# Kernel tuning notes

Hardware: AMD Instinct MI355X
Metric: run time of the kernel (lower is better)

## Reference

```python
import jax, jax.numpy as jnp
import numpy as np

DIM = 256
HEADS = 8
HEAD_DIM = DIM // HEADS
WS = 7            # window size
SHIFT = 3         # shift size
H = 56
W = 56
B = 32
WA = WS * WS      # window area = 49
NWH, NWW = H // WS, W // WS
NW = NWH * NWW    # windows per image


def _make_attn_mask():
    # replicate the torch mask construction for the shifted windows
    img = np.zeros((H, W), dtype=np.float32)
    cnt = 0
    for hs in (slice(0, -WS), slice(-WS, -SHIFT), slice(-SHIFT, None)):
        for ws_ in (slice(0, -WS), slice(-WS, -SHIFT), slice(-SHIFT, None)):
            img[hs, ws_] = cnt
            cnt += 1
    mw = img.reshape(NWH, WS, NWW, WS).transpose(0, 2, 1, 3).reshape(-1, WA)  # (nW, 49)
    diff = mw[:, None, :] - mw[:, :, None]                                    # (nW, 49, 49)
    return np.where(diff != 0, -100.0, 0.0).astype(np.float32)


def _make_rel_index():
    coords = np.stack(np.meshgrid(np.arange(WS), np.arange(WS), indexing='ij')).reshape(2, -1)
    rel = coords[:, :, None] - coords[:, None, :]        # (2, 49, 49)
    rel = rel.transpose(1, 2, 0) + (WS - 1)              # shift to >= 0
    rel[..., 0] *= 2 * WS - 1
    return rel.sum(-1).astype(np.int32)                  # (49, 49) in [0, 169)


def setup_inputs() -> dict:
    key = jax.random.key(0)
    ks = jax.random.split(key, 12)
    s = 0.02
    inp = {
        'x': jax.random.normal(ks[0], (B, H, W, DIM), dtype=jnp.float32),
        'ln1_w': jnp.ones((DIM,), jnp.float32), 'ln1_b': jnp.zeros((DIM,), jnp.float32),
        'qkv_w': s * jax.random.normal(ks[1], (3 * DIM, DIM), jnp.float32),
        'qkv_b': jnp.zeros((3 * DIM,), jnp.float32),
        'rpb_table': s * jax.random.normal(ks[2], ((2 * WS - 1) ** 2, HEADS), jnp.float32),
        'proj_w': s * jax.random.normal(ks[3], (DIM, DIM), jnp.float32),
        'proj_b': jnp.zeros((DIM,), jnp.float32),
        'ln2_w': jnp.ones((DIM,), jnp.float32), 'ln2_b': jnp.zeros((DIM,), jnp.float32),
        'fc1_w': s * jax.random.normal(ks[4], (4 * DIM, DIM), jnp.float32),
        'fc1_b': jnp.zeros((4 * DIM,), jnp.float32),
        'ln3_w': jnp.ones((4 * DIM,), jnp.float32), 'ln3_b': jnp.zeros((4 * DIM,), jnp.float32),
        'fc2_w': s * jax.random.normal(ks[5], (DIM, 4 * DIM), jnp.float32),
        'fc2_b': jnp.zeros((DIM,), jnp.float32),
        'attn_mask': jnp.asarray(_make_attn_mask()),     # (nW, 49, 49)
        'rel_index': jnp.asarray(_make_rel_index()),     # (49, 49) int32
    }
    return inp


def _ln(x, w, b, eps=1e-5):
    m = jnp.mean(x, axis=-1, keepdims=True)
    v = jnp.mean((x - m) ** 2, axis=-1, keepdims=True)
    return (x - m) * jax.lax.rsqrt(v + eps) * w + b


def reference(x, ln1_w, ln1_b, qkv_w, qkv_b, rpb_table, proj_w, proj_b,
              ln2_w, ln2_b, fc1_w, fc1_b, ln3_w, ln3_b, fc2_w, fc2_b,
              attn_mask, rel_index):
    Bn, Hn, Wn, C = x.shape
    # ---- attention branch ----
    y = _ln(x, ln1_w, ln1_b)
    sh = jnp.roll(y, (-SHIFT, -SHIFT), axis=(1, 2))
    # window partition: (B, H, W, C) -> (B*nW, 49, C)
    win = sh.reshape(Bn, NWH, WS, NWW, WS, C).transpose(0, 1, 3, 2, 4, 5).reshape(Bn * NW, WA, C)
    qkv = win @ qkv_w.T + qkv_b                              # (Bw, 49, 3C)
    qkv = qkv.reshape(Bn * NW, WA, 3, HEADS, HEAD_DIM).transpose(2, 0, 3, 1, 4)
    q, k, v = qkv[0], qkv[1], qkv[2]                         # (Bw, h, 49, d)
    scale = HEAD_DIM ** -0.5
    attn = jnp.einsum('bhqd,bhkd->bhqk', q * scale, k)       # (Bw, h, 49, 49)
    bias = rpb_table[rel_index]                              # (49, 49, h)
    attn = attn + jnp.transpose(bias, (2, 0, 1))[None]
    attn = attn.reshape(Bn, NW, HEADS, WA, WA) + attn_mask[None, :, None]
    attn = jax.nn.softmax(attn, axis=-1).reshape(Bn * NW, HEADS, WA, WA)
    out = jnp.einsum('bhqk,bhkd->bhqd', attn, v)             # (Bw, h, 49, d)
    out = out.transpose(0, 2, 1, 3).reshape(Bn * NW, WA, C)
    out = out @ proj_w.T + proj_b
    # window reverse + un-shift
    out = out.reshape(Bn, NWH, NWW, WS, WS, C).transpose(0, 1, 3, 2, 4, 5).reshape(Bn, Hn, Wn, C)
    out = jnp.roll(out, (SHIFT, SHIFT), axis=(1, 2))
    x = x + out
    # ---- MLP branch (note: extra LayerNorm inside MLP per source) ----
    z = _ln(x, ln2_w, ln2_b)
    h = jax.nn.gelu(z @ fc1_w.T + fc1_b, approximate=False)
    h = _ln(h, ln3_w, ln3_b)
    x = x + (h @ fc2_w.T + fc2_b)
    return x
```

## Files before the change

kernel.cpp:

```cpp
#include <hip/hip_runtime.h>
#include <hip/hip_bf16.h>
#include <math.h>

typedef __attribute__((ext_vector_type(8))) short bf16x8;
typedef __attribute__((ext_vector_type(4))) float f32x4;
typedef __attribute__((ext_vector_type(4))) float f4;
typedef __attribute__((ext_vector_type(8))) unsigned short us8;
typedef __attribute__((ext_vector_type(4))) unsigned short us4;
typedef unsigned short u16;
typedef unsigned int u32;

#define HEADS 8
#define SHIFT_ 3
#define HIMG 56
#define WIMG 56
#define WA 49
#define NTOK 100352
#define NPAIR 16384

static __device__ __forceinline__ float bf2f(u16 v){ return __uint_as_float(((u32)v)<<16); }
static __device__ __forceinline__ u16 f2bf(float f){
  u32 u = __float_as_uint(f);
  return (u16)((u + 0x7fffu + ((u>>16)&1u)) >> 16);
}
static __device__ __forceinline__ u32 pkbf(float a, float b){
  __hip_bfloat162 h = __float22bfloat162_rn(make_float2(a, b));
  return *reinterpret_cast<u32*>(&h);
}
static __device__ __forceinline__ float wsum(float v){
  #pragma unroll
  for (int off=32; off>0; off>>=1) v += __shfl_xor(v, off, 64);
  return v;
}
static __device__ __forceinline__ void glds16(const u16* g, u16* l){
  __builtin_amdgcn_global_load_lds(
      (const __attribute__((address_space(1))) unsigned int*)g,
      (__attribute__((address_space(3))) unsigned int*)l, 16, 0, 0);
}
static __device__ __forceinline__ int tok2pix(int row){
  int bw = row / 49, t = row - bw*49;
  int b  = bw >> 6,  w = bw & 63;
  int wh = w >> 3,   ww = w & 7;
  int th = t / 7,    tw = t - th*7;
  int r = wh*7 + th + SHIFT_; if (r >= HIMG) r -= HIMG;
  int c = ww*7 + tw + SHIFT_; if (c >= WIMG) c -= WIMG;
  return (b*HIMG + r)*WIMG + c;
}
static __device__ __forceinline__ float gelu_f(float x){
  float e = __expf(-1.702f*x);
  return x*__builtin_amdgcn_rcpf(1.0f+e);
}

__global__ void zero_kernel(float* __restrict__ p){
  p[blockIdx.x*256 + threadIdx.x] = 0.f;
}

template<int C, int ISBF>
__global__ void ln_stats_kernel(const void* __restrict__ srcv, float* __restrict__ stats){
  int wave = threadIdx.x >> 6, lane = threadIdx.x & 63;
  int tok = blockIdx.x*4 + wave;
  float s=0.f, s2=0.f;
  if (ISBF == 0){
    const float* p = (const float*)srcv + (size_t)tok*C;
    #pragma unroll
    for (int i=0;i<C/256;i++){
      f4 v = *(const f4*)(p + lane*4*(C/256) + i*4);
      #pragma unroll
      for (int e=0;e<4;e++){ float f=v[e]; s+=f; s2+=f*f; }
    }
  } else {
    const u16* p = (const u16*)srcv + (size_t)tok*C;
    #pragma unroll
    for (int i=0;i<C/512;i++){
      us8 v = *(const us8*)(p + lane*8*(C/512) + i*8);
      #pragma unroll
      for (int e=0;e<8;e++){ float f=bf2f(v[e]); s+=f; s2+=f*f; }
    }
  }
  s = wsum(s); s2 = wsum(s2);
  if (lane==0){
    float mean = s/(float)C;
    float var  = s2/(float)C - mean*mean;
    stats[2*tok]   = mean;
    stats[2*tok+1] = rsqrtf(var + 1e-5f);
  }
}

__global__ void ln_apply_kernel(const float* __restrict__ src, u16* __restrict__ dst){
  int wave = threadIdx.x >> 6, lane = threadIdx.x & 63;
  int tok = blockIdx.x*4 + wave;
  const float* p = src + (size_t)tok*256;
  f4 a = *(const f4*)(p + lane*4);
  float s = a[0]+a[1]+a[2]+a[3];
  float s2 = a[0]*a[0]+a[1]*a[1]+a[2]*a[2]+a[3]*a[3];
  s = wsum(s); s2 = wsum(s2);
  float mean = s*(1.f/256.f);
  float var  = s2*(1.f/256.f) - mean*mean;
  float rstd = rsqrtf(var + 1e-5f);
  u32 o2[2];
  o2[0] = pkbf((a[0]-mean)*rstd, (a[1]-mean)*rstd);
  o2[1] = pkbf((a[2]-mean)*rstd, (a[3]-mean)*rstd);
  *(u32*)(dst + (size_t)tok*256 + lane*4)     = o2[0];
  *(u32*)(dst + (size_t)tok*256 + lane*4 + 2) = o2[1];
}

__global__ void prep_weights(
    const float* __restrict__ qkv_w, const float* __restrict__ qkv_b,
    const float* __restrict__ ln1w,  const float* __restrict__ ln1b,
    const float* __restrict__ fc1_w, const float* __restrict__ fc1_b,
    const float* __restrict__ ln2w,  const float* __restrict__ ln2b,
    const float* __restrict__ fc2_w, const float* __restrict__ fc2_b,
    const float* __restrict__ ln3w,  const float* __restrict__ ln3b,
    const float* __restrict__ proj_w, const float* __restrict__ proj_b,
    u16* __restrict__ wq, float* __restrict__ bq,
    u16* __restrict__ w1, float* __restrict__ b1,
    u16* __restrict__ w2, float* __restrict__ b2,
    u16* __restrict__ wp, float* __restrict__ bp,
    float* __restrict__ cs2)
{
  int wave = threadIdx.x>>6, lane = threadIdx.x&63;
  int n = blockIdx.x*4 + wave;
  const float *W,*lw,*lb,*bs; u16* WO; float* BO; int K, row, noln, docs;
  if (n < 768)      { W=qkv_w; lw=ln1w; lb=ln1b; bs=qkv_b; WO=wq; BO=bq; K=256;  row=n;      noln=0; docs=0; }
  else if (n < 1792){ W=fc1_w; lw=ln2w; lb=ln2b; bs=fc1_b; WO=w1; BO=b1; K=256;  row=n-768;  noln=0; docs=0; }
  else if (n < 2048){ W=fc2_w; lw=ln3w; lb=ln3b; bs=fc2_b; WO=w2; BO=b2; K=1024; row=n-1792; noln=0; docs=1; }
  else              { W=proj_w; lw=nullptr; lb=nullptr; bs=proj_b; WO=wp; BO=bp; K=256; row=n-2048; noln=1; docs=0; }
  float dot = 0.f, cs = 0.f;
  for (int k=lane; k<K; k+=64){
    float wv = W[(size_t)row*K + k];
    if (noln){
      WO[(size_t)row*K + k] = f2bf(wv);
    } else {
      dot += wv * lb[k];
      u16 q = f2bf(wv * lw[k]);
      WO[(size_t)row*K + k] = q;
      cs += bf2f(q);
    }
  }
  dot = wsum(dot);
  if (docs){ cs = wsum(cs); if (lane==0) cs2[row] = cs; }
  if (lane==0) BO[row] = bs[row] + dot;
}

template<int SMODE, int EPI, int SWAP>
__global__ __launch_bounds__(256)
void gemm15(const void* __restrict__ Av, const u16* __restrict__ Bt,
            const float* __restrict__ stats, float* __restrict__ hstats,
            const float* __restrict__ biasf, const float* __restrict__ resid,
            const float* __restrict__ colsum, void* __restrict__ outv,
            int K, int NT, int CHUNK)
{
  constexpr int BM=128, BN=128, BK=32;
  __shared__ u16 smem[24576];
  int b = blockIdx.x;
  int linear = (b & 7)*CHUNK + (b >> 3);
  int mt = linear / NT, nt = linear - mt*NT;
  int m0 = mt*BM, n0 = nt*BN;
  int tid  = threadIdx.x;
  int lane = tid & 63, wave = tid >> 6;
  int wr = wave >> 1, wc = wave & 1;
  int lc16 = lane & 15, g = lane >> 4;
  int nsteps = K >> 5;

  const u16* asrc[2];
  const u16* bsrc[2];
  #pragma unroll
  for (int i=0;i<2;i++){
    int c = tid + i*256;
    int row = c >> 2, gch = ((c & 3) - (row >> 1)) & 3;
    if (SMODE <= 1){
      int grow = (SMODE==0) ? tok2pix(m0+row) : (m0+row);
      asrc[i] = (const u16*)Av + (size_t)grow*K + gch*8;
    }
    bsrc[i] = Bt + (size_t)(n0+row)*K + gch*8;
  }
  float smean[2], srstd[2];
  if (SMODE == 3){
    #pragma unroll
    for (int i=0;i<2;i++){
      int grow = m0 + ((tid + i*256) >> 2);
      smean[i] = stats[2*grow]; srstd[i] = stats[2*grow+1];
    }
  }

  f32x4 acc[4][4];
  #pragma unroll
  for (int i=0;i<4;i++)
    #pragma unroll
    for (int j=0;j<4;j++){ acc[i][j][0]=0.f; acc[i][j][1]=0.f; acc[i][j][2]=0.f; acc[i][j][3]=0.f; }

  if (SMODE <= 1){
    #pragma unroll
    for (int i=0;i<2;i++) glds16(asrc[i], smem + i*2048 + wave*512);
    #pragma unroll
    for (int i=0;i<2;i++) glds16(bsrc[i], smem + 12288 + i*2048 + wave*512);
    if (1 < nsteps){
      #pragma unroll
      for (int i=0;i<2;i++) glds16(asrc[i]+32, smem + 4096 + i*2048 + wave*512);
      #pragma unroll
      for (int i=0;i<2;i++) glds16(bsrc[i]+32, smem + 12288 + 4096 + i*2048 + wave*512);
      asm volatile("s_waitcnt vmcnt(4)" ::: "memory");
    } else {
      asm volatile("s_waitcnt vmcnt(0)" ::: "memory");
    }
    __builtin_amdgcn_s_barrier();

    int cur = 0;
    for (int t=0; t<nsteps; ++t){
      if (t+2 < nsteps){
        int kt2 = (t+2) << 5;
        int nb = cur + 2; if (nb >= 3) nb -= 3;
        int off = nb*4096;
        #pragma unroll
        for (int i=0;i<2;i++) glds16(asrc[i]+kt2, smem + off + i*2048 + wave*512);
        #pragma unroll
        for (int i=0;i<2;i++) glds16(bsrc[i]+kt2, smem + 12288 + off + i*2048 + wave*512);
      }
      const u16* Ap = smem + cur*4096;
      const u16* Bp = smem + 12288 + cur*4096;
      bf16x8 af[4], bfr[4];
      #pragma unroll
      for (int mi=0;mi<4;mi++){
        int r = wr*64 + mi*16 + lc16;
        u32 byte = (u32)(r*64) + ((u32)((g + (r>>1)) & 3) << 4);
        af[mi] = *(const bf16x8*)(Ap + (byte>>1));
      }
      #pragma unroll
      for (int ni=0;ni<4;ni++){
        int r = wc*64 + ni*16 + lc16;
        u32 byte = (u32)(r*64) + ((u32)((g + (r>>1)) & 3) << 4);
        bfr[ni] = *(const bf16x8*)(Bp + (byte>>1));
      }
      #pragma unroll
      for (int mi=0;mi<4;mi++)
        #pragma unroll
        for (int ni=0;ni<4;ni++)
          acc[mi][ni] = SWAP ? __builtin_amdgcn_mfma_f32_16x16x32_bf16(bfr[ni], af[mi], acc[mi][ni], 0, 0, 0)
                             : __builtin_amdgcn_mfma_f32_16x16x32_bf16(af[mi], bfr[ni], acc[mi][ni], 0, 0, 0);
      if (t+2 < nsteps)      asm volatile("s_waitcnt vmcnt(4)" ::: "memory");
      else if (t+1 < nsteps) asm volatile("s_waitcnt vmcnt(0)" ::: "memory");
      __builtin_amdgcn_s_barrier();
      cur = (cur+1 == 3) ? 0 : cur+1;
    }
  } else {
    f4 rcurf[2][2];
    #pragma unroll
    for (int i=0;i<2;i++){
      int c = tid + i*256; int row = c>>2, gch = ((c&3) - (row>>1)) & 3;
      const float* ap = (const float*)Av + (size_t)(m0+row)*K + gch*8;
      rcurf[i][0] = *(const f4*)ap; rcurf[i][1] = *(const f4*)(ap+4);
    }
    for (int t=0; t<nsteps; ++t){
      int kt = t << 5;
      #pragma unroll
      for (int i=0;i<2;i++){
        int c = tid + i*256; int row = c>>2, s = c&3;
        us8 o;
        #pragma unroll
        for (int e=0;e<8;e++){
          float fv = rcurf[i][e>>2][e&3];
          o[e] = f2bf((fv - smean[i])*srstd[i]);
        }
        u32 byte = (u32)(row*64) + ((u32)s << 4);
        *(us8*)(smem + (byte>>1)) = o;
      }
      #pragma unroll
      for (int i=0;i<2;i++) glds16(bsrc[i]+kt, smem + 12288 + i*2048 + wave*512);
      __syncthreads();
      if (t+1 < nsteps){
        int kt1 = kt + 32;
        #pragma unroll
        for (int i=0;i<2;i++){
          int c = tid + i*256; int row = c>>2, gch = ((c&3) - (row>>1)) & 3;
          const float* ap = (const float*)Av + (size_t)(m0+row)*K + kt1 + gch*8;
          rcurf[i][0] = *(const f4*)ap; rcurf[i][1] = *(const f4*)(ap+4);
        }
      }
      bf16x8 af[4], bfr[4];
      #pragma unroll
      for (int mi=0;mi<4;mi++){
        int r = wr*64 + mi*16 + lc16;
        u32 byte = (u32)(r*64) + ((u32)((g + (r>>1)) & 3) << 4);
        af[mi] = *(const bf16x8*)(smem + (byte>>1));
      }
      #pragma unroll
      for (int ni=0;ni<4;ni++){
        int r = wc*64 + ni*16 + lc16;
        u32 byte = (u32)(r*64) + ((u32)((g + (r>>1)) & 3) << 4);
        bfr[ni] = *(const bf16x8*)(smem + 12288 + (byte>>1));
      }
      #pragma unroll
      for (int mi=0;mi<4;mi++)
        #pragma unroll
        for (int ni=0;ni<4;ni++)
          acc[mi][ni] = SWAP ? __builtin_amdgcn_mfma_f32_16x16x32_bf16(bfr[ni], af[mi], acc[mi][ni], 0, 0, 0)
                             : __builtin_amdgcn_mfma_f32_16x16x32_bf16(af[mi], bfr[ni], acc[mi][ni], 0, 0, 0);
      __syncthreads();
    }
  }

  int lr = lane >> 4;
  if (EPI==0){
    u16* Cs = smem;
    #pragma unroll
    for (int mi=0;mi<4;mi++){
      #pragma unroll
      for (int ni=0;ni<4;ni++){
        int cl = wc*64 + ni*16 + lc16;
        float bv = biasf[n0 + cl];
        #pragma unroll
        for (int j=0;j<4;j++){
          int rl = wr*64 + mi*16 + lr*4 + j;
          float v = acc[mi][ni][j] + bv;
          u32 byte = (u32)(rl*256 + cl*2) ^ ((u32)(rl&7)<<4);
          Cs[byte>>1] = f2bf(v);
        }
      }
    }
    __syncthreads();
    #pragma unroll
    for (int i=0;i<8;i++){
      int c = tid + i*256;
      int rl = c>>4, c0 = (c&15)*8;
      u32 byte = (u32)(rl*256 + c0*2) ^ ((u32)(rl&7)<<4);
      us8 v = *(const us8*)(Cs + (byte>>1));
      int row = m0 + rl, col = n0 + c0;
      int which = col>>8, hh = (col>>5)&7, d0 = col&31;
      int bwi = row/49, t = row - bwi*49;
      *(us8*)((u16*)outv + ((size_t)which*NPAIR + bwi*8 + hh)*(WA*32) + t*32 + d0) = v;
    }
  } else if (EPI==2){
    u16* Cs = smem;
    #pragma unroll
    for (int mi=0;mi<4;mi++){
      int rl = wr*64 + mi*16 + lc16;
      float ss = 0.f, sq = 0.f;
      #pragma unroll
      for (int ni=0;ni<4;ni++){
        int cl = wc*64 + ni*16 + g*4;
        f4 bv = *(const f4*)(biasf + n0 + cl);
        float v0 = gelu_f(acc[mi][ni][0] + bv[0]);
        float v1 = gelu_f(acc[mi][ni][1] + bv[1]);
        float v2 = gelu_f(acc[mi][ni][2] + bv[2]);
        float v3 = gelu_f(acc[mi][ni][3] + bv[3]);
        ss += (v0+v1)+(v2+v3);
        sq += (v0*v0+v1*v1)+(v2*v2+v3*v3);
        u32 w0 = pkbf(v0, v1), w1 = pkbf(v2, v3);
        u32 byte = (u32)(rl*256 + cl*2) ^ ((u32)(rl&7)<<4);
        *(u32*)(Cs + (byte>>1))     = w0;
        *(u32*)(Cs + (byte>>1) + 2) = w1;
      }
      ss += __shfl_xor(ss, 16, 64); ss += __shfl_xor(ss, 32, 64);
      sq += __shfl_xor(sq, 16, 64); sq += __shfl_xor(sq, 32, 64);
      if (g==0){
        int grow = m0 + rl;
        atomicAdd(&hstats[2*grow],   ss);
        atomicAdd(&hstats[2*grow+1], sq);
      }
    }
    __syncthreads();
    #pragma unroll
    for (int i=0;i<8;i++){
      int c = tid + i*256;
      int rl = c>>4, c0 = (c&15)*8;
      u32 byte = (u32)(rl*256 + c0*2) ^ ((u32)(rl&7)<<4);
      us8 v = *(const us8*)(Cs + (byte>>1));
      int row = m0 + rl, col = n0 + c0;
      *(us8*)((u16*)outv + (size_t)row*1024 + col) = v;
    }
  } else {
    #pragma unroll
    for (int mi=0;mi<4;mi++){
      int rl = wr*64 + mi*16 + lc16;
      int grow = m0 + rl;
      float rs = 1.f, mr = 0.f;
      if (EPI==4){
        float s = stats[2*grow], q = stats[2*grow+1];
        float mean = s*(1.f/1024.f);
        float var  = q*(1.f/1024.f) - mean*mean;
        rs = rsqrtf(var + 1e-5f);
        mr = mean*rs;
      }
      size_t rowbase = (EPI==1) ? (size_t)tok2pix(grow)*256 : (size_t)grow*256;
      #pragma unroll
      for (int ni=0;ni<4;ni++){
        int col = n0 + wc*64 + ni*16 + g*4;
        f4 bv = *(const f4*)(biasf + col);
        f4 v;
        if (EPI==4){
          f4 cw = *(const f4*)(colsum + col);
          #pragma unroll
          for (int j=0;j<4;j++) v[j] = acc[mi][ni][j]*rs - mr*cw[j] + bv[j];
        } else {
          #pragma unroll
          for (int j=0;j<4;j++) v[j] = acc[mi][ni][j] + bv[j];
        }
        f4 rr = *(const f4*)(resid + rowbase + col);
        v += rr;
        *(f4*)((float*)outv + rowbase + col) = v;
      }
    }
  }
}

__global__ void attn_mfma_kernel(
    const u16* __restrict__ qkv,
    const float* __restrict__ rpb,
    const int* __restrict__ rel,
    const float* __restrict__ mask,
    u16* __restrict__ outb)
{
  __shared__ u16 Kls[4][64*32];
  __shared__ u16 Vt [4][32*64];
  __shared__ u16 Pls[4][64*64];
  int wave = threadIdx.x>>6, lane = threadIdx.x&63;
  int pair = blockIdx.x*4 + wave;
  int bw = pair>>3, h = pair&7, w = bw&63;
  int lc = lane&15, g = lane>>4;
  const u16* qg = qkv + (size_t)pair*(WA*32);
  const u16* kg = qg + (size_t)NPAIR*(WA*32);
  const u16* vg = qg + (size_t)2*NPAIR*(WA*32);
  u16* Kp = &Kls[wave][0];
  u16* Vp = &Vt[wave][0];
  u16* Pp = &Pls[wave][0];

  #pragma unroll
  for (int i=0;i<4;i++){
    int idx = i*64 + lane;
    int r = idx>>2, seg = idx&3;
    us8 kv, vv;
    if (r < WA){
      kv = *(const us8*)(kg + r*32 + seg*8);
      vv = *(const us8*)(vg + r*32 + seg*8);
    } else {
      #pragma unroll
      for (int e=0;e<8;e++){ kv[e]=0; vv[e]=0; }
    }
    *(us8*)(Kp + r*32 + seg*8) = kv;
    #pragma unroll
    for (int e=0;e<8;e++){
      int d = seg*8 + e;
      u32 byte = ((u32)(d*128 + r*2)) ^ ((u32)(d&7)<<4);
      Vp[byte>>1] = vv[e];
    }
  }

  bf16x8 qa[4];
  #pragma unroll
  for (int mi=0;mi<4;mi++){
    int r = mi*16 + lc;
    if (r < WA) qa[mi] = *(const bf16x8*)(qg + r*32 + g*8);
    else { bf16x8 z;
           #pragma unroll
           for (int e=0;e<8;e++) z[e]=0; qa[mi]=z; }
  }

  f32x4 acc[4][4];
  #pragma unroll
  for (int i=0;i<4;i++)
    #pragma unroll
    for (int j=0;j<4;j++){ acc[i][j][0]=0.f; acc[i][j][1]=0.f; acc[i][j][2]=0.f; acc[i][j][3]=0.f; }
  __syncthreads();
  __builtin_amdgcn_s_setprio(1);
  #pragma unroll
  for (int ni=0;ni<4;ni++){
    bf16x8 kb = *(const bf16x8*)(Kp + (ni*16+lc)*32 + g*8);
    #pragma unroll
    for (int mi=0;mi<4;mi++)
      acc[mi][ni] = __builtin_amdgcn_mfma_f32_16x16x32_bf16(qa[mi], kb, acc[mi][ni], 0, 0, 0);
  }
  __builtin_amdgcn_s_setprio(0);

  const float scale = 0.17677669529663689f;
  float rinv[4][4];
  #pragma unroll
  for (int mi=0;mi<4;mi++){
    #pragma unroll
    for (int jr=0;jr<4;jr++){
      int i = mi*16 + g*4 + jr;
      float sv[4];
      #pragma unroll
      for (int ni=0;ni<4;ni++){
        int j = ni*16 + lc;
        float s;
        if (i < WA && j < WA){
          s = acc[mi][ni][jr]*scale + rpb[rel[i*WA+j]*8 + h] + mask[((size_t)w*WA + i)*WA + j];
        } else s = -1e9f;
        sv[ni] = s;
      }
      float mx = fmaxf(fmaxf(sv[0],sv[1]), fmaxf(sv[2],sv[3]));
      #pragma unroll
      for (int off=1; off<16; off<<=1) mx = fmaxf(mx, __shfl_xor(mx, off, 64));
      float sum = 0.f;
      #pragma unroll
      for (int ni=0;ni<4;ni++){ sv[ni] = __expf(sv[ni]-mx); sum += sv[ni]; }
      #pragma unroll
      for (int off=1; off<16; off<<=1) sum += __shfl_xor(sum, off, 64);
      rinv[mi][jr] = __builtin_amdgcn_rcpf(sum);
      #pragma unroll
      for (int ni=0;ni<4;ni++){
        int j = ni*16 + lc;
        u32 byte = ((u32)(i*128 + j*2)) ^ ((u32)(i&7)<<4);
        Pp[byte>>1] = f2bf(sv[ni]);
      }
    }
  }

  bf16x8 vb[2][2];
  #pragma unroll
  for (int kk=0;kk<2;kk++)
    #pragma unroll
    for (int ni=0;ni<2;ni++){
      int d = ni*16 + lc;
      u32 byte = ((u32)(d*128 + kk*64 + g*16)) ^ ((u32)(d&7)<<4);
      vb[kk][ni] = *(const bf16x8*)(Vp + (byte>>1));
    }
  f32x4 aco[4][2];
  #pragma unroll
  for (int i=0;i<4;i++)
    #pragma unroll
    for (int j=0;j<2;j++){ aco[i][j][0]=0.f; aco[i][j][1]=0.f; aco[i][j][2]=0.f; aco[i][j][3]=0.f; }
  __builtin_amdgcn_s_setprio(1);
  #pragma unroll
  for (int mi=0;mi<4;mi++){
    int r = mi*16 + lc;
    #pragma unroll
    for (int kk=0;kk<2;kk++){
      u32 byte = ((u32)(r*128 + kk*64 + g*16)) ^ ((u32)(r&7)<<4);
      bf16x8 pa = *(const bf16x8*)(Pp + (byte>>1));
      #pragma unroll
      for (int ni=0;ni<2;ni++)
        aco[mi][ni] = __builtin_amdgcn_mfma_f32_16x16x32_bf16(pa, vb[kk][ni], aco[mi][ni], 0, 0, 0);
    }
  }
  __builtin_amdgcn_s_setprio(0);

  u16* Op = Kp;
  #pragma unroll
  for (int mi=0;mi<4;mi++){
    #pragma unroll
    for (int jr=0;jr<4;jr++){
      int i = mi*16 + g*4 + jr;
      if (i < WA){
        float rv = rinv[mi][jr];
        #pragma unroll
        for (int ni=0;ni<2;ni++)
          Op[i*32 + ni*16 + lc] = f2bf(aco[mi][ni][jr]*rv);
      }
    }
  }
  __syncthreads();
  size_t obase = (size_t)(bw*WA)*256 + h*32;
  #pragma unroll
  for (int i=0;i<4;i++){
    int c = i*64 + lane;
    if (c < WA*4){
      int t = c>>2, seg = c&3;
      *(us8*)(outb + obase + (size_t)t*256 + seg*8) = *(const us8*)(Op + t*32 + seg*8);
    }
  }
}

extern "C" void kernel_launch(void* const* d_in, const int* in_sizes, int n_in,
                              void* d_out, int out_size, void* d_ws, size_t ws_size,
                              hipStream_t stream) {
  const float* x      = (const float*)d_in[0];
  const float* ln1w   = (const float*)d_in[1];
  const float* ln1b   = (const float*)d_in[2];
  const float* qkv_w  = (const float*)d_in[3];
  const float* qkv_b  = (const float*)d_in[4];
  const float* rpb    = (const float*)d_in[5];
  const float* proj_w = (const float*)d_in[6];
  const float* proj_b = (const float*)d_in[7];
  const float* ln2w   = (const float*)d_in[8];
  const float* ln2b   = (const float*)d_in[9];
  const float* fc1_w  = (const float*)d_in[10];
  const float* fc1_b  = (const float*)d_in[11];
  const float* ln3w   = (const float*)d_in[12];
  const float* ln3b   = (const float*)d_in[13];
  const float* fc2_w  = (const float*)d_in[14];
  const float* fc2_b  = (const float*)d_in[15];
  const float* amask  = (const float*)d_in[16];
  const int*   rel    = (const int*)d_in[17];
  float* out = (float*)d_out;

  char* ws = (char*)d_ws;
  float* hstats = (float*)(ws);
  float* statsB = (float*)(ws +  802816);
  float* bq     = (float*)(ws + 1605632);
  float* b1     = (float*)(ws + 1608704);
  float* b2     = (float*)(ws + 1612800);
  float* bp     = (float*)(ws + 1613824);
  float* cs2    = (float*)(ws + 1614848);
  u16*   wq     = (u16*)  (ws + 1615872);
  u16*   w1     = (u16*)  (ws + 2009088);
  u16*   w2     = (u16*)  (ws + 2533376);
  u16*   wp     = (u16*)  (ws + 3057664);
  const size_t P0 = 3188736;
  u16*   qkvbuf = (u16*)(ws + P0);
  u16*   attno  = (u16*)(ws + P0 + 154140672);
  u16*   xb     = (u16*)(ws + P0 + 154140672);
  u16*   hbuf   = (u16*)(ws + P0);
  u16*   x1b    = (u16*)(ws + P0 + 205520896);
  const int bigws = (ws_size >= (size_t)(P0 + 205520896ull + 51380224ull));

  prep_weights<<<576,256,0,stream>>>(qkv_w,qkv_b,ln1w,ln1b, fc1_w,fc1_b,ln2w,ln2b,
                                     fc2_w,fc2_b,ln3w,ln3b, proj_w,proj_b,
                                     wq,bq, w1,b1, w2,b2, wp,bp, cs2);
  ln_apply_kernel<<<NTOK/4,256,0,stream>>>(x, xb);
  gemm15<0,0,0><<<784*6,256,0,stream>>>(xb, wq, nullptr, nullptr, bq, nullptr, nullptr, qkvbuf, 256, 6, 588);
  attn_mfma_kernel<<<NPAIR/4,256,0,stream>>>(qkvbuf, rpb, rel, amask, attno);
  gemm15<1,1,1><<<784*2,256,0,stream>>>(attno, wp, nullptr, nullptr, bp, x, nullptr, out, 256, 2, 196);
  zero_kernel<<<784,256,0,stream>>>(hstats);
  if (bigws){
    ln_apply_kernel<<<NTOK/4,256,0,stream>>>(out, x1b);
    gemm15<1,2,1><<<784*8,256,0,stream>>>(x1b, w1, nullptr, hstats, b1, nullptr, nullptr, hbuf, 256, 8, 784);
  } else {
    ln_stats_kernel<256,0><<<NTOK/4,256,0,stream>>>(out, statsB);
    gemm15<3,2,1><<<784*8,256,0,stream>>>(out, w1, statsB, hstats, b1, nullptr, nullptr, hbuf, 256, 8, 784);
  }
  gemm15<1,4,1><<<784*2,256,0,stream>>>(hbuf, w2, hstats, nullptr, b2, out, cs2, out, 1024, 2, 196);
}
```

Measured before the change: 561.0 us.

## Store post-attention residual as bf16 and rebuild it from LN output in fc2

The proj GEMM now writes the residual stream as bf16 into a scratch buffer instead of fp32 to the output. A new LN kernel reads the bf16 values and saves per-token mean and rstd. The fc2 epilogue then reconstructs the residual from the normalized bf16 x1b as x = xn/rstd + mean, so it no longer needs an fp32 residual read. This removes fp32 residual write and read traffic, at the cost of bf16 rounding on the residual path, which lowers output accuracy.

```diff
diff --git a/kernel.cpp b/kernel.cpp
--- a/kernel.cpp
+++ b/kernel.cpp
@@ -102,6 +102,27 @@
   o2[1] = pkbf((a[2]-mean)*rstd, (a[3]-mean)*rstd);
   *(u32*)(dst + (size_t)tok*256 + lane*4)     = o2[0];
   *(u32*)(dst + (size_t)tok*256 + lane*4 + 2) = o2[1];
+}
+
+__global__ void ln_apply_b_kernel(const u16* __restrict__ src, u16* __restrict__ dst,
+                                  float* __restrict__ st){
+  int wave = threadIdx.x >> 6, lane = threadIdx.x & 63;
+  int tok = blockIdx.x*4 + wave;
+  const u16* p = src + (size_t)tok*256 + lane*4;
+  us4 a4 = *(const us4*)p;
+  float a0=bf2f(a4[0]), a1=bf2f(a4[1]), a2=bf2f(a4[2]), a3=bf2f(a4[3]);
+  float s = a0+a1+a2+a3;
+  float s2 = a0*a0+a1*a1+a2*a2+a3*a3;
+  s = wsum(s); s2 = wsum(s2);
+  float mean = s*(1.f/256.f);
+  float var  = s2*(1.f/256.f) - mean*mean;
+  float rstd = rsqrtf(var + 1e-5f);
+  u32 o0 = pkbf((a0-mean)*rstd, (a1-mean)*rstd);
+  u32 o1 = pkbf((a2-mean)*rstd, (a3-mean)*rstd);
+  u16* d = dst + (size_t)tok*256 + lane*4;
+  *(u32*)d     = o0;
+  *(u32*)(d+2) = o1;
+  if (lane==0){ st[2*tok] = mean; st[2*tok+1] = rstd; }
 }
 
 __global__ void prep_weights(
@@ -144,7 +165,7 @@
 
 template<int SMODE, int EPI, int SWAP>
 __global__ __launch_bounds__(256)
-void gemm15(const void* __restrict__ Av, const u16* __restrict__ Bt,
+void gemm17(const void* __restrict__ Av, const u16* __restrict__ Bt,
             const float* __restrict__ stats, float* __restrict__ hstats,
             const float* __restrict__ biasf, const float* __restrict__ resid,
             const float* __restrict__ colsum, void* __restrict__ outv,
@@ -368,26 +389,62 @@
       int row = m0 + rl, col = n0 + c0;
       *(us8*)((u16*)outv + (size_t)row*1024 + col) = v;
     }
+  } else if (EPI==5){
+    u16* Cs = smem;
+    #pragma unroll
+    for (int mi=0;mi<4;mi++){
+      int rl = wr*64 + mi*16 + lc16;
+      int pix = tok2pix(m0 + rl);
+      #pragma unroll
+      for (int ni=0;ni<4;ni++){
+        int cl = wc*64 + ni*16 + g*4;
+        int col = n0 + cl;
+        f4 bv = *(const f4*)(biasf + col);
+        f4 rr = *(const f4*)(resid + (size_t)pix*256 + col);
+        float v0 = acc[mi][ni][0] + bv[0] + rr[0];
+        float v1 = acc[mi][ni][1] + bv[1] + rr[1];
+        float v2 = acc[mi][ni][2] + bv[2] + rr[2];
+        float v3 = acc[mi][ni][3] + bv[3] + rr[3];
+        u32 w0 = pkbf(v0, v1), w1 = pkbf(v2, v3);
+        u32 byte = (u32)(rl*256 + cl*2) ^ ((u32)(rl&7)<<4);
+        *(u32*)(Cs + (byte>>1))     = w0;
+        *(u32*)(Cs + (byte>>1) + 2) = w1;
+      }
+    }
+    __syncthreads();
+    #pragma unroll
+    for (int i=0;i<8;i++){
+      int c = tid + i*256;
+      int rl = c>>4, c0 = (c&15)*8;
+      u32 byte = (u32)(rl*256 + c0*2) ^ ((u32)(rl&7)<<4);
+      us8 v = *(const us8*)(Cs + (byte>>1));
+      int pix = tok2pix(m0 + rl);
+      *(us8*)((u16*)outv + (size_t)pix*256 + n0 + c0) = v;
+    }
   } else {
     #pragma unroll
     for (int mi=0;mi<4;mi++){
       int rl = wr*64 + mi*16 + lc16;
       int grow = m0 + rl;
-      float rs = 1.f, mr = 0.f;
-      if (EPI==4){
+      float rs = 1.f, mr = 0.f, istd2 = 0.f, mean2 = 0.f;
+      if (EPI==4 || EPI==6){
         float s = stats[2*grow], q = stats[2*grow+1];
         float mean = s*(1.f/1024.f);
         float var  = q*(1.f/1024.f) - mean*mean;
         rs = rsqrtf(var + 1e-5f);
         mr = mean*rs;
       }
+      if (EPI==6){
+        mean2 = hstats[2*grow];
+        istd2 = __builtin_amdgcn_rcpf(hstats[2*grow+1]);
+      }
       size_t rowbase = (EPI==1) ? (size_t)tok2pix(grow)*256 : (size_t)grow*256;
       #pragma unroll
       for (int ni=0;ni<4;ni++){
         int col = n0 + wc*64 + ni*16 + g*4;
         f4 bv = *(const f4*)(biasf + col);
         f4 v;
-        if (EPI==4){
+        if (EPI==4 || EPI==6){
           f4 cw = *(const f4*)(colsum + col);
           #pragma unroll
           for (int j=0;j<4;j++) v[j] = acc[mi][ni][j]*rs - mr*cw[j] + bv[j];
@@ -395,8 +452,14 @@
           #pragma unroll
           for (int j=0;j<4;j++) v[j] = acc[mi][ni][j] + bv[j];
         }
-        f4 rr = *(const f4*)(resid + rowbase + col);
-        v += rr;
+        if (EPI==6){
+          us4 xr = *(const us4*)((const u16*)resid + rowbase + col);
+          #pragma unroll
+          for (int j=0;j<4;j++) v[j] += bf2f(xr[j])*istd2 + mean2;
+        } else {
+          f4 rr = *(const f4*)(resid + rowbase + col);
+          v += rr;
+        }
         *(f4*)((float*)outv + rowbase + col) = v;
       }
     }
@@ -586,7 +649,7 @@
 
   char* ws = (char*)d_ws;
   float* hstats = (float*)(ws);
-  float* statsB = (float*)(ws +  802816);
+  float* stats2 = (float*)(ws +  802816);
   float* bq     = (float*)(ws + 1605632);
   float* b1     = (float*)(ws + 1608704);
   float* b2     = (float*)(ws + 1612800);
@@ -600,6 +663,7 @@
   u16*   qkvbuf = (u16*)(ws + P0);
   u16*   attno  = (u16*)(ws + P0 + 154140672);
   u16*   xb     = (u16*)(ws + P0 + 154140672);
+  u16*   ob     = (u16*)(ws + P0);
   u16*   hbuf   = (u16*)(ws + P0);
   u16*   x1b    = (u16*)(ws + P0 + 205520896);
   const int bigws = (ws_size >= (size_t)(P0 + 205520896ull + 51380224ull));
@@ -608,16 +672,18 @@
                                      fc2_w,fc2_b,ln3w,ln3b, proj_w,proj_b,
                                      wq,bq, w1,b1, w2,b2, wp,bp, cs2);
   ln_apply_kernel<<<NTOK/4,256,0,stream>>>(x, xb);
-  gemm15<0,0,0><<<784*6,256,0,stream>>>(xb, wq, nullptr, nullptr, bq, nullptr, nullptr, qkvbuf, 256, 6, 588);
+  gemm17<0,0,0><<<784*6,256,0,stream>>>(xb, wq, nullptr, nullptr, bq, nullptr, nullptr, qkvbuf, 256, 6, 588);
   attn_mfma_kernel<<<NPAIR/4,256,0,stream>>>(qkvbuf, rpb, rel, amask, attno);
-  gemm15<1,1,1><<<784*2,256,0,stream>>>(attno, wp, nullptr, nullptr, bp, x, nullptr, out, 256, 2, 196);
   zero_kernel<<<784,256,0,stream>>>(hstats);
   if (bigws){
-    ln_apply_kernel<<<NTOK/4,256,0,stream>>>(out, x1b);
-    gemm15<1,2,1><<<784*8,256,0,stream>>>(x1b, w1, nullptr, hstats, b1, nullptr, nullptr, hbuf, 256, 8, 784);
+    gemm17<1,5,1><<<784*2,256,0,stream>>>(attno, wp, nullptr, nullptr, bp, x, nullptr, ob, 256, 2, 196);
+    ln_apply_b_kernel<<<NTOK/4,256,0,stream>>>(ob, x1b, stats2);
+    gemm17<1,2,1><<<784*8,256,0,stream>>>(x1b, w1, nullptr, hstats, b1, nullptr, nullptr, hbuf, 256, 8, 784);
+    gemm17<1,6,1><<<784*2,256,0,stream>>>(hbuf, w2, hstats, stats2, b2, (const float*)x1b, cs2, out, 1024, 2, 196);
   } else {
-    ln_stats_kernel<256,0><<<NTOK/4,256,0,stream>>>(out, statsB);
-    gemm15<3,2,1><<<784*8,256,0,stream>>>(out, w1, statsB, hstats, b1, nullptr, nullptr, hbuf, 256, 8, 784);
-  }
-  gemm15<1,4,1><<<784*2,256,0,stream>>>(hbuf, w2, hstats, nullptr, b2, out, cs2, out, 1024, 2, 196);
-}
+    gemm17<1,1,1><<<784*2,256,0,stream>>>(attno, wp, nullptr, nullptr, bp, x, nullptr, out, 256, 2, 196);
+    ln_stats_kernel<256,0><<<NTOK/4,256,0,stream>>>(out, stats2);
+    gemm17<3,2,1><<<784*8,256,0,stream>>>(out, w1, stats2, hstats, b1, nullptr, nullptr, (u16*)(ws+P0), 256, 8, 784);
+    gemm17<1,4,1><<<784*2,256,0,stream>>>((u16*)(ws+P0), w2, hstats, nullptr, b2, out, cs2, out, 1024, 2, 196);
+  }
+}
```

Result: faster. 531.9 us (-5.2%).
